# Performance work log

Hardware: AMD Instinct MI355X
Metric: run time of the kernel (lower is better)

The kernel has to match this reference:

```python
import jax, jax.numpy as jnp
import numpy as np

IIR_LEN = 16384


def _causal_fft_conv(x, h):
    # x: (B, T), h: (B, K); causal conv truncated to first T samples
    T = x.shape[-1]
    K = h.shape[-1]
    fft_n = 1 << int(np.ceil(np.log2(T + K - 1)))
    X = jnp.fft.rfft(x, fft_n)
    H = jnp.fft.rfft(h, fft_n)
    y = jnp.fft.irfft(X * H, fft_n)
    return y[..., :T]


def setup_inputs() -> dict:
    key = jax.random.key(0)
    k1, k2 = jax.random.split(key)
    signal = jax.random.normal(k1, (32, 2, 131072), dtype=jnp.float32)
    z_alpha = jax.random.normal(k2, (32, 1), dtype=jnp.float32)
    return {"signal": signal, "z_alpha": z_alpha}


def reference(signal, z_alpha):
    alpha = jnp.clip(jax.nn.sigmoid(z_alpha), 1e-5, 1.0 - 1e-5)          # (B, 1)
    energy = jnp.mean(jnp.square(signal), axis=-2)                       # (B, T)
    arange = jnp.arange(IIR_LEN, dtype=jnp.float32)[None, :]             # (1, K)
    decay = jnp.exp(arange * jnp.log(alpha))                             # (B, K)
    h = (1.0 - alpha) * decay                                            # (B, K)
    envelope = jax.nn.relu(_causal_fft_conv(energy, h))                  # (B, T)
    return jnp.log(envelope + 1e-5)
```

## Files before the change

### kernel.cpp

```cpp
#include <hip/hip_runtime.h>
#include <math.h>

#define T_LEN   131072
#define CHUNK   16384
#define EPT     32
#define NT      1024

__global__ __launch_bounds__(NT) void iir_env_kernel(
    const float* __restrict__ signal,
    const float* __restrict__ z_alpha,
    float* __restrict__ out)
{
    __shared__ float sbuf[16384];

    const int tid  = threadIdx.x;
    const int lane = tid & 63;
    const int wid  = tid >> 6;
    const int bid  = blockIdx.x;
    const int row  = bid >> 3;
    const int chk  = bid & 7;

    double zd = (double)z_alpha[row];
    double ad = 1.0 / (1.0 + exp(-zd));
    ad = ad < 1e-5 ? 1e-5 : (ad > (1.0 - 1e-5) ? (1.0 - 1e-5) : ad);
    const float a     = (float)ad;
    const float onema = (float)(1.0 - ad);
    double p = ad;
    p = p*p; p = p*p; p = p*p; p = p*p; p = p*p;
    const float A32 = (float)p;
    p = p*p; p = p*p; p = p*p; p = p*p; p = p*p; p = p*p;
    const float A2048 = (float)p;
    p = p*p; p = p*p; p = p*p;
    const float aK = (float)p;

    const int gbase = (chk - 1) * CHUNK + tid * EPT;
    const float* p0 = signal + (size_t)row * 2 * T_LEN;
    const float* p1 = p0 + T_LEN;

    float e[EPT];
    if (gbase >= 0) {
        #pragma unroll
        for (int k = 0; k < EPT/4; ++k) {
            const float4 x0 = *reinterpret_cast<const float4*>(p0 + gbase + 4*k);
            const float4 x1 = *reinterpret_cast<const float4*>(p1 + gbase + 4*k);
            e[4*k+0] = 0.5f * fmaf(x0.x, x0.x, x1.x*x1.x);
            e[4*k+1] = 0.5f * fmaf(x0.y, x0.y, x1.y*x1.y);
            e[4*k+2] = 0.5f * fmaf(x0.z, x0.z, x1.z*x1.z);
            e[4*k+3] = 0.5f * fmaf(x0.w, x0.w, x1.w*x1.w);
        }
    } else {
        #pragma unroll
        for (int i = 0; i < EPT; ++i) e[i] = 0.0f;
    }

    float s0 = 0.0f;
    #pragma unroll
    for (int i = 0; i < EPT; ++i) s0 = fmaf(a, s0, onema * e[i]);

    float v = s0;
    float m = A32;
    #pragma unroll
    for (int off = 1; off < 64; off <<= 1) {
        float up = __shfl_up(v, off, 64);
        if (lane >= off) v = fmaf(m, up, v);
        m = m * m;
    }
    if (lane == 63) sbuf[wid] = v;
    __syncthreads();

    float P = 0.0f;
    for (int w = 0; w < wid; ++w) P = fmaf(A2048, P, sbuf[w]);

    float iprev = __shfl_up(v, 1, 64);
    float apl = 1.0f, bb = A32;
    #pragma unroll
    for (int b = 0; b < 6; ++b) { if (lane & (1 << b)) apl *= bb; bb = bb * bb; }
    const float E = fmaf(apl, P, (lane > 0) ? iprev : 0.0f);

    __syncthreads();

    if (tid < NT/2) {
        float st = E;
        #pragma unroll
        for (int i = 0; i < EPT; ++i) {
            st = fmaf(a, st, onema * e[i]);
            sbuf[tid * EPT + (i ^ (tid & 31))] = st;
        }
    }
    __syncthreads();

    if (tid >= NT/2) {
        const int rr = tid - NT/2;
        float st = E;
        float* po = out + (size_t)row * T_LEN + chk * CHUNK + rr * EPT;
        #pragma unroll
        for (int k = 0; k < EPT/4; ++k) {
            float4 o;
            float* ov = &o.x;
            #pragma unroll
            for (int j = 0; j < 4; ++j) {
                const int i = 4*k + j;
                st = fmaf(a, st, onema * e[i]);
                float y = fmaf(-aK, sbuf[rr * EPT + (i ^ (rr & 31))], st);
                ov[j] = logf(fmaxf(y, 0.0f) + 1e-5f);
            }
            *reinterpret_cast<float4*>(po + 4*k) = o;
        }
    }
}

extern "C" void kernel_launch(void* const* d_in, const int* in_sizes, int n_in,
                              void* d_out, int out_size, void* d_ws, size_t ws_size,
                              hipStream_t stream) {
    const float* signal  = (const float*)d_in[0];
    const float* z_alpha = (const float*)d_in[1];
    float* out = (float*)d_out;
    dim3 grid(32 * 8);
    dim3 block(NT);
    hipLaunchKernelGGL(iir_env_kernel, grid, block, 0, stream, signal, z_alpha, out);
}
```

Before: 90.78 us.

## Shrink chunk to 8K with 16K history window, skip loads for negligible decay

```diff
diff --git a/kernel.cpp b/kernel.cpp
--- a/kernel.cpp
+++ b/kernel.cpp
@@ -1,48 +1,61 @@
 #include <hip/hip_runtime.h>
 #include <math.h>
 
-#define T_LEN   131072
-#define CHUNK   16384
-#define EPT     32
-#define NT      1024
+#define T_LEN  131072
+#define HIST   16384
+#define CHUNK  8192
+#define WIN    (HIST + CHUNK)
+#define EPT    32
+#define NT     (WIN / EPT)
+#define NWAVE  (NT / 64)
+#define OUT_T0 (HIST / EPT)
+#define PARK_T (CHUNK / EPT)
 
 __global__ __launch_bounds__(NT) void iir_env_kernel(
     const float* __restrict__ signal,
     const float* __restrict__ z_alpha,
     float* __restrict__ out)
 {
-    __shared__ float sbuf[16384];
+    __shared__ float park[CHUNK];
+    __shared__ float carr[NWAVE];
 
     const int tid  = threadIdx.x;
     const int lane = tid & 63;
     const int wid  = tid >> 6;
-    const int bid  = blockIdx.x;
-    const int row  = bid >> 3;
-    const int chk  = bid & 7;
+    const int row  = blockIdx.x >> 4;
+    const int chk  = blockIdx.x & 15;
 
     double zd = (double)z_alpha[row];
     double ad = 1.0 / (1.0 + exp(-zd));
-    ad = ad < 1e-5 ? 1e-5 : (ad > (1.0 - 1e-5) ? (1.0 - 1e-5) : ad);
+    ad = ad < 1e-5 ? 1e-5 : (ad > 1.0 - 1e-5 ? 1.0 - 1e-5 : ad);
     const float a     = (float)ad;
     const float onema = (float)(1.0 - ad);
+    const double Hd   = 18.42 / (-log(ad));
+    const bool  needK = (Hd >= (double)HIST);
+    const int   Hint  = needK ? HIST : (int)Hd + 1;
+
     double p = ad;
     p = p*p; p = p*p; p = p*p; p = p*p; p = p*p;
     const float A32 = (float)p;
     p = p*p; p = p*p; p = p*p; p = p*p; p = p*p; p = p*p;
     const float A2048 = (float)p;
-    p = p*p; p = p*p; p = p*p;
-    const float aK = (float)p;
+    float aK = 0.0f;
+    if (needK) { double q = p; q = q*q; q = q*q; q = q*q; aK = (float)q; }
 
-    const int gbase = (chk - 1) * CHUNK + tid * EPT;
-    const float* p0 = signal + (size_t)row * 2 * T_LEN;
+    const int wpos   = tid * EPT;
+    const int t0     = chk * CHUNK;
+    const int gstart = t0 - HIST + wpos;
+    const bool loadOK = (gstart >= 0) && (wpos + EPT > HIST - Hint);
+
+    const float* p0 = signal + (size_t)row * 2 * T_LEN + gstart;
     const float* p1 = p0 + T_LEN;
 
     float e[EPT];
-    if (gbase >= 0) {
+    if (loadOK) {
         #pragma unroll
         for (int k = 0; k < EPT/4; ++k) {
-            const float4 x0 = *reinterpret_cast<const float4*>(p0 + gbase + 4*k);
-            const float4 x1 = *reinterpret_cast<const float4*>(p1 + gbase + 4*k);
+            const float4 x0 = *reinterpret_cast<const float4*>(p0 + 4*k);
+            const float4 x1 = *reinterpret_cast<const float4*>(p1 + 4*k);
             e[4*k+0] = 0.5f * fmaf(x0.x, x0.x, x1.x*x1.x);
             e[4*k+1] = 0.5f * fmaf(x0.y, x0.y, x1.y*x1.y);
             e[4*k+2] = 0.5f * fmaf(x0.z, x0.z, x1.z*x1.z);
@@ -65,34 +78,34 @@
         if (lane >= off) v = fmaf(m, up, v);
         m = m * m;
     }
-    if (lane == 63) sbuf[wid] = v;
+    if (lane == 63) carr[wid] = v;
     __syncthreads();
 
     float P = 0.0f;
-    for (int w = 0; w < wid; ++w) P = fmaf(A2048, P, sbuf[w]);
+    for (int w = 0; w < wid; ++w) P = fmaf(A2048, P, carr[w]);
 
-    float iprev = __shfl_up(v, 1, 64);
+    const float iprev = __shfl_up(v, 1, 64);
     float apl = 1.0f, bb = A32;
     #pragma unroll
     for (int b = 0; b < 6; ++b) { if (lane & (1 << b)) apl *= bb; bb = bb * bb; }
     const float E = fmaf(apl, P, (lane > 0) ? iprev : 0.0f);
 
-    __syncthreads();
+    if (needK) {
+        if (tid < PARK_T) {
+            float st = E;
+            #pragma unroll
+            for (int i = 0; i < EPT; ++i) {
+                st = fmaf(a, st, onema * e[i]);
+                park[wpos + (i ^ (tid & 31))] = st;
+            }
+        }
+        __syncthreads();
+    }
 
-    if (tid < NT/2) {
+    if (tid >= OUT_T0) {
+        const int rr = tid - OUT_T0;
         float st = E;
-        #pragma unroll
-        for (int i = 0; i < EPT; ++i) {
-            st = fmaf(a, st, onema * e[i]);
-            sbuf[tid * EPT + (i ^ (tid & 31))] = st;
-        }
-    }
-    __syncthreads();
-
-    if (tid >= NT/2) {
-        const int rr = tid - NT/2;
-        float st = E;
-        float* po = out + (size_t)row * T_LEN + chk * CHUNK + rr * EPT;
+        float* po = out + (size_t)row * T_LEN + t0 + rr * EPT;
         #pragma unroll
         for (int k = 0; k < EPT/4; ++k) {
             float4 o;
@@ -101,8 +114,9 @@
             for (int j = 0; j < 4; ++j) {
                 const int i = 4*k + j;
                 st = fmaf(a, st, onema * e[i]);
-                float y = fmaf(-aK, sbuf[rr * EPT + (i ^ (rr & 31))], st);
-                ov[j] = logf(fmaxf(y, 0.0f) + 1e-5f);
+                float y = st;
+                if (needK) y = fmaf(-aK, park[rr * EPT + (i ^ (rr & 31))], st);
+                ov[j] = __logf(fmaxf(y, 0.0f) + 1e-5f);
             }
             *reinterpret_cast<float4*>(po + 4*k) = o;
         }
@@ -115,7 +129,7 @@
     const float* signal  = (const float*)d_in[0];
     const float* z_alpha = (const float*)d_in[1];
     float* out = (float*)d_out;
-    dim3 grid(32 * 8);
+    dim3 grid(32 * (T_LEN / CHUNK));
     dim3 block(NT);
     hipLaunchKernelGGL(iir_env_kernel, grid, block, 0, stream, signal, z_alpha, out);
 }
```

After: 84.06 us. 1.08x faster.
